# Kernel optimization log

Hardware: AMD Instinct MI355X
Metric: run time of the kernel (lower is better)

The kernel has to match this reference:

```python
import jax, jax.numpy as jnp
import numpy as np

BATCH, SEQ_LEN, VEC_DIM, WIDTH = 64, 256, 512, 3


def setup_inputs() -> dict:
    key = jax.random.key(0)
    k = jax.random.split(key, 8)
    F0r = jax.random.normal(k[0], (BATCH, SEQ_LEN, VEC_DIM), jnp.float32)
    F1r = jax.random.normal(k[1], (BATCH, SEQ_LEN, VEC_DIM), jnp.float32)
    sent0_mask = (jax.random.uniform(k[2], (BATCH, SEQ_LEN)) < 0.9).astype(jnp.float32)
    sent1_mask = (jax.random.uniform(k[3], (BATCH, SEQ_LEN)) < 0.9).astype(jnp.float32)
    # nn.Parameter(torch.randn(seq_len, vec_dim))
    W0 = jax.random.normal(k[4], (SEQ_LEN, VEC_DIM), jnp.float32)
    W1 = jax.random.normal(k[5], (SEQ_LEN, VEC_DIM), jnp.float32)
    # Conv2d(2, 1, kernel_size=(WIDTH, 1)) default init: U(-1/sqrt(fan_in), +)
    bound = 1.0 / np.sqrt(2 * WIDTH * 1)
    conv_w = jax.random.uniform(k[6], (1, 2, WIDTH, 1), jnp.float32, -bound, bound)
    conv_b = jax.random.uniform(k[7], (1,), jnp.float32, -bound, bound)
    return dict(F0r=F0r, F1r=F1r, sent0_mask=sent0_mask, sent1_mask=sent1_mask,
                W0=W0, W1=W1, conv_w=conv_w, conv_b=conv_b)


def _conv_tanh_pool(x, conv_w, conv_b):
    # x: [B, 2, S, D]; conv pad (WIDTH-1, 0) -> [B, 1, S+WIDTH-1, D]
    y = jax.lax.conv_general_dilated(
        x, conv_w, window_strides=(1, 1),
        padding=((WIDTH - 1, WIDTH - 1), (0, 0)),
        dimension_numbers=('NCHW', 'OIHW', 'NCHW'))
    y = jnp.tanh(y + conv_b[None, :, None, None])
    # AvgPool2d kernel (WIDTH,1), stride 1 -> [B, 1, S, D]
    y = jax.lax.reduce_window(y, 0.0, jax.lax.add,
                              (1, 1, WIDTH, 1), (1, 1, 1, 1), 'VALID') / WIDTH
    return y[:, 0]  # squeeze channel -> [B, S, D]


def reference(F0r, F1r, sent0_mask, sent1_mask, W0, W1, conv_w, conv_b):
    # masking is in-place in the torch code, so masked F0/F1 feed the conv too
    F0 = F0r * sent0_mask[:, :, None]  # [B, S, D]
    F1 = F1r * sent1_mask[:, :, None]
    # pairwise L2 via ||u-v||^2 = ||u||^2 + ||v||^2 - 2 u.v (avoids [B,S,S,D])
    sq0 = jnp.sum(F0 * F0, axis=-1)  # [B, S]
    sq1 = jnp.sum(F1 * F1, axis=-1)
    cross = jnp.einsum('bid,bjd->bij', F0, F1)  # [B, S, S]
    d2 = jnp.maximum(sq0[:, :, None] + sq1[:, None, :] - 2.0 * cross, 0.0)
    norm = jnp.where(d2 > 0, jnp.sqrt(jnp.where(d2 > 0, d2, 1.0)), 0.0)
    A = 1.0 / (1.0 + norm)  # [B, S, S]
    F0a = jnp.einsum('bij,id->bjd', A, W0)  # A^T @ W0
    F1a = jnp.einsum('bij,jd->bid', A, W1)  # A @ W1
    x0 = jnp.stack([F0, F0a], axis=1)  # [B, 2, S, D]
    x1 = jnp.stack([F1, F1a], axis=1)
    out0 = _conv_tanh_pool(x0, conv_w, conv_b)
    out1 = _conv_tanh_pool(x1, conv_w, conv_b)
    return out0, out1
```

## Files before the change

### kernel.cpp

```cpp
#include <hip/hip_runtime.h>

typedef unsigned short u16;
typedef __attribute__((ext_vector_type(8))) short short8;
typedef __attribute__((ext_vector_type(4))) float f32x4;

__device__ inline u16 f2bf(float f) {
    union { float f; unsigned u; } v; v.f = f;
    unsigned u = v.u;
    unsigned r = (u + 0x7FFFu + ((u >> 16) & 1u)) >> 16;
    return (u16)r;
}
__device__ inline float bf2f(u16 h) {
    union { unsigned u; float f; } v; v.u = ((unsigned)h) << 16;
    return v.f;
}
__device__ inline float ftanh(float x) {
    float e = __expf(2.f * x);
    return 1.f - 2.f / (e + 1.f);
}
__device__ inline float4 bf4f(ushort4 u) {
    float4 f; f.x = bf2f(u.x); f.y = bf2f(u.y); f.z = bf2f(u.z); f.w = bf2f(u.w);
    return f;
}

__global__ __launch_bounds__(128) void prep_kernel(
    const float* __restrict__ F0r, const float* __restrict__ F1r,
    const float* __restrict__ m0, const float* __restrict__ m1,
    const float* __restrict__ W0, const float* __restrict__ W1,
    u16* __restrict__ F0b, u16* __restrict__ F1b,
    u16* __restrict__ WT0, u16* __restrict__ WT1,
    float* __restrict__ sq0, float* __restrict__ sq1)
{
    int bx = blockIdx.x;
    int t = threadIdx.x;
    if (bx >= 16384) {
        int idx = (bx - 16384) * 128 + t;
        int a = idx >> 17;
        int r = idx & 131071;
        int s = r >> 9, d = r & 511;
        const float* W = a ? W1 : W0;
        u16* WT = a ? WT1 : WT0;
        WT[d * 256 + s] = f2bf(W[r]);
        return;
    }
    int bs = bx;
    size_t base = (size_t)bs * 512 + t * 4;
    float mk0 = m0[bs], mk1 = m1[bs];
    float4 v0 = *(const float4*)(F0r + base);
    float4 v1 = *(const float4*)(F1r + base);
    v0.x *= mk0; v0.y *= mk0; v0.z *= mk0; v0.w *= mk0;
    v1.x *= mk1; v1.y *= mk1; v1.z *= mk1; v1.w *= mk1;
    ushort4 u0; u0.x = f2bf(v0.x); u0.y = f2bf(v0.y); u0.z = f2bf(v0.z); u0.w = f2bf(v0.w);
    ushort4 u1; u1.x = f2bf(v1.x); u1.y = f2bf(v1.y); u1.z = f2bf(v1.z); u1.w = f2bf(v1.w);
    *(ushort4*)(F0b + base) = u0;
    *(ushort4*)(F1b + base) = u1;
    float s0p = v0.x*v0.x + v0.y*v0.y + v0.z*v0.z + v0.w*v0.w;
    float s1p = v1.x*v1.x + v1.y*v1.y + v1.z*v1.z + v1.w*v1.w;
    #pragma unroll
    for (int off = 32; off > 0; off >>= 1) {
        s0p += __shfl_xor(s0p, off);
        s1p += __shfl_xor(s1p, off);
    }
    __shared__ float red0[2], red1[2];
    if ((t & 63) == 0) { red0[t >> 6] = s0p; red1[t >> 6] = s1p; }
    __syncthreads();
    if (t == 0) { sq0[bs] = red0[0] + red0[1]; sq1[bs] = red1[0] + red1[1]; }
}

__global__ __launch_bounds__(256) void gemm_cross_kernel(
    const u16* __restrict__ F0b, const u16* __restrict__ F1b,
    const float* __restrict__ sq0, const float* __restrict__ sq1,
    u16* __restrict__ Abf, u16* __restrict__ ATbf)
{
    __shared__ __align__(16) u16 smem[64 * 136 * 2];
    u16 (*As)[136] = (u16(*)[136])smem;
    u16 (*Bs)[136] = (u16(*)[136])(smem + 64 * 136);

    int b = blockIdx.y;
    int i0 = (blockIdx.x >> 2) * 64, j0 = (blockIdx.x & 3) * 64;
    const u16* Ap = F0b + (size_t)b * 131072;
    const u16* Bp = F1b + (size_t)b * 131072;
    const float* sqR = sq0 + b * 256;
    const float* sqC = sq1 + b * 256;

    const int t = threadIdx.x;
    const int lane = t & 63, w = t >> 6;
    const int wm = w >> 1, wn = w & 1;
    const int q = lane >> 4, lm = lane & 15;

    f32x4 acc[2][2];
    #pragma unroll
    for (int x = 0; x < 2; ++x)
        #pragma unroll
        for (int y = 0; y < 2; ++y)
            acc[x][y] = (f32x4){0.f, 0.f, 0.f, 0.f};

    for (int k0 = 0; k0 < 512; k0 += 128) {
        #pragma unroll
        for (int i = 0; i < 4; ++i) {
            int idx = i * 256 + t;
            int row = idx >> 4;
            int seg = idx & 15;
            *(uint4*)&As[row][seg * 8] =
                *(const uint4*)(Ap + (size_t)(i0 + row) * 512 + k0 + seg * 8);
            *(uint4*)&Bs[row][seg * 8] =
                *(const uint4*)(Bp + (size_t)(j0 + row) * 512 + k0 + seg * 8);
        }
        __syncthreads();
        #pragma unroll
        for (int ks = 0; ks < 128; ks += 32) {
            short8 af[2], bfr[2];
            #pragma unroll
            for (int x = 0; x < 2; ++x) {
                af[x]  = *(const short8*)&As[wm * 32 + x * 16 + lm][ks + q * 8];
                bfr[x] = *(const short8*)&Bs[wn * 32 + x * 16 + lm][ks + q * 8];
            }
            #pragma unroll
            for (int x = 0; x < 2; ++x)
                #pragma unroll
                for (int y = 0; y < 2; ++y)
                    acc[x][y] = __builtin_amdgcn_mfma_f32_16x16x32_bf16(
                        af[x], bfr[y], acc[x][y], 0, 0, 0);
        }
        __syncthreads();
    }

    u16 (*Ct)[136] = (u16(*)[136])smem;
    #pragma unroll
    for (int x = 0; x < 2; ++x) {
        #pragma unroll
        for (int r = 0; r < 4; ++r) {
            int ir = wm * 32 + x * 16 + q * 4 + r;
            float si = sqR[i0 + ir];
            #pragma unroll
            for (int y = 0; y < 2; ++y) {
                int jc = wn * 32 + y * 16 + lm;
                float d2 = si + sqC[j0 + jc] - 2.f * acc[x][y][r];
                d2 = fmaxf(d2, 0.f);
                float a = 1.f / (1.f + sqrtf(d2));
                Ct[ir][jc] = f2bf(a);
            }
        }
    }
    __syncthreads();

    u16* Aout  = Abf  + (size_t)b * 65536;
    u16* ATout = ATbf + (size_t)b * 65536;
    int ii = t >> 2;
    int c0 = (t & 3) * 16;
    #pragma unroll
    for (int c = 0; c < 4; ++c) {
        ushort4 v = *(ushort4*)&Ct[ii][c0 + c * 4];
        *(ushort4*)&Aout[(size_t)(i0 + ii) * 256 + j0 + c0 + c * 4] = v;
    }
    #pragma unroll
    for (int c = 0; c < 4; ++c) {
        ushort4 v;
        v.x = Ct[c0 + c * 4 + 0][ii];
        v.y = Ct[c0 + c * 4 + 1][ii];
        v.z = Ct[c0 + c * 4 + 2][ii];
        v.w = Ct[c0 + c * 4 + 3][ii];
        *(ushort4*)&ATout[(size_t)(j0 + ii) * 256 + i0 + c0 + c * 4] = v;
    }
}

__global__ __launch_bounds__(256) void fa_conv_kernel(
    const u16* __restrict__ Abf, const u16* __restrict__ ATbf,
    const u16* __restrict__ WT0, const u16* __restrict__ WT1,
    const u16* __restrict__ F0b, const u16* __restrict__ F1b,
    const float* __restrict__ cw, const float* __restrict__ cb,
    float* __restrict__ out)
{
    __shared__ __align__(16) u16 Al[48][264];
    __shared__ __align__(16) u16 Bl[128][72];
    __shared__ __align__(16) u16 Fl[36][132];

    int b = blockIdx.y, side = blockIdx.z;
    int s0 = blockIdx.x * 32;
    const u16* Ap = (side ? Abf : ATbf) + (size_t)b * 65536;
    const u16* WT = side ? WT1 : WT0;
    const u16* Fb = (side ? F1b : F0b) + (size_t)b * 131072;
    float* o = out + (size_t)side * 8388608 + (size_t)b * 131072;

    const int t = threadIdx.x;
    const int lane = t & 63, w = t >> 6;
    const int q = lane >> 4, lm = lane & 15;

    #pragma unroll
    for (int i = 0; i < 6; ++i) {
        int idx = i * 256 + t;
        int r = idx >> 5;
        int seg = idx & 31;
        int s = s0 - 2 + r;
        uint4 v = {0u, 0u, 0u, 0u};
        if (r < 36 && (unsigned)s < 256u)
            v = *(const uint4*)(Ap + (size_t)s * 256 + seg * 8);
        *(uint4*)&Al[r][seg * 8] = v;
    }

    float w00 = cw[0], w01 = cw[1], w02 = cw[2];
    float w10 = cw[3], w11 = cw[4], w12 = cw[5];
    float bias = cb[0];
    const float third = 1.f / 3.f;
    const int g = t >> 5;
    const int dl = (t & 31) * 4;

    for (int n0 = 0; n0 < 512; n0 += 128) {
        f32x4 acc[3][2];
        #pragma unroll
        for (int x = 0; x < 3; ++x)
            #pragma unroll
            for (int y = 0; y < 2; ++y)
                acc[x][y] = (f32x4){0.f, 0.f, 0.f, 0.f};

        for (int kb = 0; kb < 256; kb += 64) {
            #pragma unroll
            for (int i = 0; i < 4; ++i) {
                int idx = i * 256 + t;
                int r = idx >> 3;
                int seg = idx & 7;
                *(uint4*)&Bl[r][seg * 8] =
                    *(const uint4*)(WT + (size_t)(n0 + r) * 256 + kb + seg * 8);
            }
            __syncthreads();
            #pragma unroll
            for (int ks = 0; ks < 64; ks += 32) {
                short8 af[3], bfr[2];
                #pragma unroll
                for (int x = 0; x < 3; ++x)
                    af[x] = *(const short8*)&Al[x * 16 + lm][kb + ks + q * 8];
                #pragma unroll
                for (int y = 0; y < 2; ++y)
                    bfr[y] = *(const short8*)&Bl[w * 32 + y * 16 + lm][ks + q * 8];
                #pragma unroll
                for (int x = 0; x < 3; ++x)
                    #pragma unroll
                    for (int y = 0; y < 2; ++y)
                        acc[x][y] = __builtin_amdgcn_mfma_f32_16x16x32_bf16(
                            af[x], bfr[y], acc[x][y], 0, 0, 0);
            }
            __syncthreads();
        }

        #pragma unroll
        for (int x = 0; x < 3; ++x)
            #pragma unroll
            for (int r = 0; r < 4; ++r) {
                int m = x * 16 + q * 4 + r;
                if (m < 36) {
                    #pragma unroll
                    for (int y = 0; y < 2; ++y)
                        Fl[m][w * 32 + y * 16 + lm] = f2bf(acc[x][y][r]);
                }
            }
        __syncthreads();

        float4 f[8], a[8];
        #pragma unroll
        for (int k = 0; k < 8; ++k) {
            int s = s0 + g * 4 - 2 + k;
            if ((unsigned)s < 256u)
                f[k] = bf4f(*(const ushort4*)(Fb + (size_t)s * 512 + n0 + dl));
            else
                f[k] = make_float4(0.f, 0.f, 0.f, 0.f);
            a[k] = bf4f(*(const ushort4*)&Fl[g * 4 + k][dl]);
        }
        float4 ty[6];
        #pragma unroll
        for (int k = 0; k < 6; ++k) {
            float4 y;
            y.x = bias + w00*f[k].x + w01*f[k+1].x + w02*f[k+2].x + w10*a[k].x + w11*a[k+1].x + w12*a[k+2].x;
            y.y = bias + w00*f[k].y + w01*f[k+1].y + w02*f[k+2].y + w10*a[k].y + w11*a[k+1].y + w12*a[k+2].y;
            y.z = bias + w00*f[k].z + w01*f[k+1].z + w02*f[k+2].z + w10*a[k].z + w11*a[k+1].z + w12*a[k+2].z;
            y.w = bias + w00*f[k].w + w01*f[k+1].w + w02*f[k+2].w + w10*a[k].w + w11*a[k+1].w + w12*a[k+2].w;
            y.x = ftanh(y.x); y.y = ftanh(y.y); y.z = ftanh(y.z); y.w = ftanh(y.w);
            ty[k] = y;
        }
        #pragma unroll
        for (int r = 0; r < 4; ++r) {
            float4 res;
            res.x = (ty[r].x + ty[r+1].x + ty[r+2].x) * third;
            res.y = (ty[r].y + ty[r+1].y + ty[r+2].y) * third;
            res.z = (ty[r].z + ty[r+1].z + ty[r+2].z) * third;
            res.w = (ty[r].w + ty[r+1].w + ty[r+2].w) * third;
            *(float4*)(o + (size_t)(s0 + g * 4 + r) * 512 + n0 + dl) = res;
        }
        __syncthreads();
    }
}

extern "C" void kernel_launch(void* const* d_in, const int* in_sizes, int n_in,
                              void* d_out, int out_size, void* d_ws, size_t ws_size,
                              hipStream_t stream)
{
    const float* F0r = (const float*)d_in[0];
    const float* F1r = (const float*)d_in[1];
    const float* m0  = (const float*)d_in[2];
    const float* m1  = (const float*)d_in[3];
    const float* W0  = (const float*)d_in[4];
    const float* W1  = (const float*)d_in[5];
    const float* cw  = (const float*)d_in[6];
    const float* cb  = (const float*)d_in[7];
    float* out = (float*)d_out;

    char* ws = (char*)d_ws;
    u16* F0b   = (u16*)(ws);
    u16* F1b   = (u16*)(ws + 16777216);
    u16* Abf   = (u16*)(ws + 33554432);
    u16* ATbf  = (u16*)(ws + 41943040);
    float* sq0 = (float*)(ws + 50331648);
    float* sq1 = (float*)(ws + 50397184);
    u16* WT0   = (u16*)(ws + 50462720);
    u16* WT1   = (u16*)(ws + 50724864);

    prep_kernel<<<18432, 128, 0, stream>>>(F0r, F1r, m0, m1, W0, W1,
                                           F0b, F1b, WT0, WT1, sq0, sq1);
    gemm_cross_kernel<<<dim3(16, 64), 256, 0, stream>>>(F0b, F1b, sq0, sq1, Abf, ATbf);
    fa_conv_kernel<<<dim3(8, 64, 2), 256, 0, stream>>>(Abf, ATbf, WT0, WT1,
                                                       F0b, F1b, cw, cb, out);
}
```

Measured before the change: 201.6 us.

## Register-prefetch global tiles and shrink LDS footprint in both GEMM kernels

Both GEMM kernels now issue the next K-tile's global loads into registers before computing on the current LDS tile, so global latency overlaps MFMA work. The conv kernel also trims the A tile to 36 rows, aliases the B tile and the F staging buffer in one LDS array, prefetches the F rows early, and sets launch_bounds min blocks to 4 to raise occupancy. In exchange it uses more registers per thread and relies on careful barrier placement around the aliased LDS buffer.

```diff
diff --git a/kernel.cpp b/kernel.cpp
--- a/kernel.cpp
+++ b/kernel.cpp
@@ -95,16 +95,29 @@
         for (int y = 0; y < 2; ++y)
             acc[x][y] = (f32x4){0.f, 0.f, 0.f, 0.f};
 
+    uint4 ar[4], br[4];
+    #pragma unroll
+    for (int i = 0; i < 4; ++i) {
+        int idx = i * 256 + t, row = idx >> 4, seg = idx & 15;
+        ar[i] = *(const uint4*)(Ap + (size_t)(i0 + row) * 512 + seg * 8);
+        br[i] = *(const uint4*)(Bp + (size_t)(j0 + row) * 512 + seg * 8);
+    }
+
     for (int k0 = 0; k0 < 512; k0 += 128) {
+        if (k0) __syncthreads();
         #pragma unroll
         for (int i = 0; i < 4; ++i) {
-            int idx = i * 256 + t;
-            int row = idx >> 4;
-            int seg = idx & 15;
-            *(uint4*)&As[row][seg * 8] =
-                *(const uint4*)(Ap + (size_t)(i0 + row) * 512 + k0 + seg * 8);
-            *(uint4*)&Bs[row][seg * 8] =
-                *(const uint4*)(Bp + (size_t)(j0 + row) * 512 + k0 + seg * 8);
+            int idx = i * 256 + t, row = idx >> 4, seg = idx & 15;
+            *(uint4*)&As[row][seg * 8] = ar[i];
+            *(uint4*)&Bs[row][seg * 8] = br[i];
+        }
+        if (k0 + 128 < 512) {
+            #pragma unroll
+            for (int i = 0; i < 4; ++i) {
+                int idx = i * 256 + t, row = idx >> 4, seg = idx & 15;
+                ar[i] = *(const uint4*)(Ap + (size_t)(i0 + row) * 512 + (k0 + 128) + seg * 8);
+                br[i] = *(const uint4*)(Bp + (size_t)(j0 + row) * 512 + (k0 + 128) + seg * 8);
+            }
         }
         __syncthreads();
         #pragma unroll
@@ -122,8 +135,8 @@
                     acc[x][y] = __builtin_amdgcn_mfma_f32_16x16x32_bf16(
                         af[x], bfr[y], acc[x][y], 0, 0, 0);
         }
-        __syncthreads();
-    }
+    }
+    __syncthreads();
 
     u16 (*Ct)[136] = (u16(*)[136])smem;
     #pragma unroll
@@ -164,16 +177,17 @@
     }
 }
 
-__global__ __launch_bounds__(256) void fa_conv_kernel(
+__global__ __launch_bounds__(256, 4) void fa_conv_kernel(
     const u16* __restrict__ Abf, const u16* __restrict__ ATbf,
     const u16* __restrict__ WT0, const u16* __restrict__ WT1,
     const u16* __restrict__ F0b, const u16* __restrict__ F1b,
     const float* __restrict__ cw, const float* __restrict__ cb,
     float* __restrict__ out)
 {
-    __shared__ __align__(16) u16 Al[48][264];
-    __shared__ __align__(16) u16 Bl[128][72];
-    __shared__ __align__(16) u16 Fl[36][132];
+    __shared__ __align__(16) u16 Al[36][264];
+    __shared__ __align__(16) u16 BlFl[128 * 72];
+    u16 (*Bl)[72]  = (u16(*)[72])BlFl;
+    u16 (*Fl)[132] = (u16(*)[132])BlFl;
 
     int b = blockIdx.y, side = blockIdx.z;
     int s0 = blockIdx.x * 32;
@@ -187,16 +201,23 @@
     const int q = lane >> 4, lm = lane & 15;
 
     #pragma unroll
-    for (int i = 0; i < 6; ++i) {
+    for (int i = 0; i < 5; ++i) {
         int idx = i * 256 + t;
-        int r = idx >> 5;
-        int seg = idx & 31;
-        int s = s0 - 2 + r;
-        uint4 v = {0u, 0u, 0u, 0u};
-        if (r < 36 && (unsigned)s < 256u)
-            v = *(const uint4*)(Ap + (size_t)s * 256 + seg * 8);
-        *(uint4*)&Al[r][seg * 8] = v;
-    }
+        if (idx < 1152) {
+            int r = idx >> 5;
+            int seg = idx & 31;
+            int s = s0 - 2 + r;
+            uint4 v = {0u, 0u, 0u, 0u};
+            if ((unsigned)s < 256u)
+                v = *(const uint4*)(Ap + (size_t)s * 256 + seg * 8);
+            *(uint4*)&Al[r][seg * 8] = v;
+        }
+    }
+
+    const u16* aRow[3];
+    aRow[0] = &Al[lm][0];
+    aRow[1] = &Al[16 + lm][0];
+    aRow[2] = &Al[(lm < 4) ? (32 + lm) : 0][0];
 
     float w00 = cw[0], w01 = cw[1], w02 = cw[2];
     float w10 = cw[3], w11 = cw[4], w12 = cw[5];
@@ -205,7 +226,23 @@
     const int g = t >> 5;
     const int dl = (t & 31) * 4;
 
+    uint4 brg[4];
+    #pragma unroll
+    for (int i = 0; i < 4; ++i) {
+        int idx = i * 256 + t, r = idx >> 3, seg = idx & 7;
+        brg[i] = *(const uint4*)(WT + (size_t)r * 256 + seg * 8);
+    }
+
     for (int n0 = 0; n0 < 512; n0 += 128) {
+        ushort4 frg[8];
+        #pragma unroll
+        for (int k = 0; k < 8; ++k) {
+            int s = s0 + g * 4 - 2 + k;
+            ushort4 z = {0, 0, 0, 0};
+            frg[k] = ((unsigned)s < 256u)
+                   ? *(const ushort4*)(Fb + (size_t)s * 512 + n0 + dl) : z;
+        }
+
         f32x4 acc[3][2];
         #pragma unroll
         for (int x = 0; x < 3; ++x)
@@ -214,13 +251,18 @@
                 acc[x][y] = (f32x4){0.f, 0.f, 0.f, 0.f};
 
         for (int kb = 0; kb < 256; kb += 64) {
+            __syncthreads();
             #pragma unroll
             for (int i = 0; i < 4; ++i) {
-                int idx = i * 256 + t;
-                int r = idx >> 3;
-                int seg = idx & 7;
-                *(uint4*)&Bl[r][seg * 8] =
-                    *(const uint4*)(WT + (size_t)(n0 + r) * 256 + kb + seg * 8);
+                int idx = i * 256 + t, r = idx >> 3, seg = idx & 7;
+                *(uint4*)&Bl[r][seg * 8] = brg[i];
+            }
+            if (kb < 192) {
+                #pragma unroll
+                for (int i = 0; i < 4; ++i) {
+                    int idx = i * 256 + t, r = idx >> 3, seg = idx & 7;
+                    brg[i] = *(const uint4*)(WT + (size_t)(n0 + r) * 256 + (kb + 64) + seg * 8);
+                }
             }
             __syncthreads();
             #pragma unroll
@@ -228,7 +270,7 @@
                 short8 af[3], bfr[2];
                 #pragma unroll
                 for (int x = 0; x < 3; ++x)
-                    af[x] = *(const short8*)&Al[x * 16 + lm][kb + ks + q * 8];
+                    af[x] = *(const short8*)(aRow[x] + kb + ks + q * 8);
                 #pragma unroll
                 for (int y = 0; y < 2; ++y)
                     bfr[y] = *(const short8*)&Bl[w * 32 + y * 16 + lm][ks + q * 8];
@@ -239,8 +281,8 @@
                         acc[x][y] = __builtin_amdgcn_mfma_f32_16x16x32_bf16(
                             af[x], bfr[y], acc[x][y], 0, 0, 0);
             }
-            __syncthreads();
-        }
+        }
+        __syncthreads();
 
         #pragma unroll
         for (int x = 0; x < 3; ++x)
@@ -253,16 +295,19 @@
                         Fl[m][w * 32 + y * 16 + lm] = f2bf(acc[x][y][r]);
                 }
             }
+        if (n0 < 384) {
+            #pragma unroll
+            for (int i = 0; i < 4; ++i) {
+                int idx = i * 256 + t, r = idx >> 3, seg = idx & 7;
+                brg[i] = *(const uint4*)(WT + (size_t)(n0 + 128 + r) * 256 + seg * 8);
+            }
+        }
         __syncthreads();
 
         float4 f[8], a[8];
         #pragma unroll
         for (int k = 0; k < 8; ++k) {
-            int s = s0 + g * 4 - 2 + k;
-            if ((unsigned)s < 256u)
-                f[k] = bf4f(*(const ushort4*)(Fb + (size_t)s * 512 + n0 + dl));
-            else
-                f[k] = make_float4(0.f, 0.f, 0.f, 0.f);
+            f[k] = bf4f(frg[k]);
             a[k] = bf4f(*(const ushort4*)&Fl[g * 4 + k][dl]);
         }
         float4 ty[6];
@@ -285,7 +330,6 @@
             res.w = (ty[r].w + ty[r+1].w + ty[r+2].w) * third;
             *(float4*)(o + (size_t)(s0 + g * 4 + r) * 512 + n0 + dl) = res;
         }
-        __syncthreads();
     }
 }
 
```

Measured after the change: 256.2 us. +27.1%, slower.
